# Kernel optimization log

Measured on AMD Instinct MI355X. Metric: run time of the kernel, lower is better.

Reference implementation:

```python
import jax, jax.numpy as jnp
import numpy as np
import math

DIM = 1024
H = 16
D = 64
M = 64  # num_features
B = 1
N = 2048


def _orf_omega(key):
    # Orthogonal Random Features: stack Q^T blocks from QR of Gaussian [D,D]
    blocks = []
    n_blocks = (M + D - 1) // D
    for i in range(n_blocks):
        G = jax.random.normal(jax.random.fold_in(key, i), (D, D), dtype=jnp.float32)
        Q, _ = jnp.linalg.qr(G)
        blocks.append(Q.T)
    return jnp.concatenate(blocks, axis=0)[:M]  # [M, D]


def setup_inputs() -> dict:
    key = jax.random.key(0)
    ks = jax.random.split(key, 7)
    inner = H * D
    x = jax.random.normal(ks[0], (B, N, DIM), dtype=jnp.float32)
    omega = _orf_omega(ks[1])
    wq = jax.random.normal(ks[2], (inner, DIM), dtype=jnp.float32) * 0.02
    wk = jax.random.normal(ks[3], (inner, DIM), dtype=jnp.float32) * 0.02
    wv = jax.random.normal(ks[4], (inner, DIM), dtype=jnp.float32) * 0.02
    wo = jax.random.normal(ks[5], (DIM, inner), dtype=jnp.float32) * 0.02
    bo = jnp.zeros((DIM,), dtype=jnp.float32)
    return {"x": x, "omega": omega, "wq": wq, "wk": wk, "wv": wv, "wo": wo, "bo": bo}


def _phi(x, omega):
    # x: [B,H,N,D], omega: [M,D] -> [B,H,N,M]
    proj = jnp.einsum('bhnd,md->bhnm', x, omega)
    norm = 0.5 * jnp.sum(x * x, axis=-1, keepdims=True)
    return jnp.exp(proj - norm) / math.sqrt(M)


def _heads(t):
    b, n, _ = t.shape
    return t.reshape(b, n, H, D).transpose(0, 2, 1, 3)  # [B,H,N,D]


def reference(x, omega, wq, wk, wv, wo, bo):
    b, n, _ = x.shape
    q = _heads(x @ wq.T)
    k = _heads(x @ wk.T)
    v = _heads(x @ wv.T)
    phi_q = _phi(q, omega)  # [B,H,N,M]
    phi_k = _phi(k, omega)
    # causal linear attention: cumulative KV state (naive materialization, faithful to source)
    kv = jnp.einsum('bhnm,bhnd->bhnmd', phi_k, v)       # [B,H,N,M,D]
    kv_cumsum = jnp.cumsum(kv, axis=2)
    k_cumsum = jnp.cumsum(phi_k, axis=2)                # [B,H,N,M]
    out = jnp.einsum('bhnm,bhnmd->bhnd', phi_q, kv_cumsum)
    z = 1.0 / (jnp.einsum('bhnm,bhnm->bhn', phi_q, k_cumsum) + 1e-6)
    out = out * z[..., None]
    out = out.transpose(0, 2, 1, 3).reshape(b, n, H * D)
    return out @ wo.T + bo
```

## Files before the change

kernel.cpp:

```cpp
#include <hip/hip_runtime.h>
#include <hip/hip_bf16.h>

typedef __hip_bfloat16 bf16;
typedef __attribute__((ext_vector_type(8))) short bf16x8;
typedef __attribute__((ext_vector_type(8))) _Float16 f16x8;
typedef __attribute__((ext_vector_type(4))) float f32x4;

constexpr int N_TOK = 2048;
constexpr int DIMM  = 1024;
constexpr int NH    = 16;
constexpr int HD    = 64;
constexpr int FM    = 64;
constexpr int NC    = 32;
constexpr int CS    = 64;

__device__ __forceinline__ float b2f(bf16 v) { return __bfloat162float(v); }
__device__ __forceinline__ unsigned short f2bfu(float v) {
  bf16 h = __float2bfloat16(v);
  return *reinterpret_cast<unsigned short*>(&h);
}
__device__ __forceinline__ unsigned short f2hu(float v) {
  _Float16 h = (_Float16)v;
  return *reinterpret_cast<unsigned short*>(&h);
}

__device__ __forceinline__ void gl_lds16(const void* g, short* l) {
  __builtin_amdgcn_global_load_lds(
      (const __attribute__((address_space(1))) void*)g,
      (__attribute__((address_space(3))) void*)l, 16, 0, 0);
}

__device__ __forceinline__ void split_pack_bf(const float4 v, uint2& ph, uint2& pl) {
  float f[4] = {v.x, v.y, v.z, v.w};
  unsigned short h[4], l[4];
  #pragma unroll
  for (int j = 0; j < 4; j++) {
    bf16 hb = __float2bfloat16(f[j]);
    h[j] = *reinterpret_cast<unsigned short*>(&hb);
    l[j] = f2bfu(f[j] - b2f(hb));
  }
  ph.x = (unsigned)h[0] | ((unsigned)h[1] << 16);
  ph.y = (unsigned)h[2] | ((unsigned)h[3] << 16);
  pl.x = (unsigned)l[0] | ((unsigned)l[1] << 16);
  pl.y = (unsigned)l[2] | ((unsigned)l[3] << 16);
}

__global__ __launch_bounds__(256) void cvt_all(
    const float4* __restrict__ x, const float4* __restrict__ wq,
    const float4* __restrict__ wk, const float4* __restrict__ wv,
    const float4* __restrict__ wo,
    _Float16* __restrict__ x16, _Float16* __restrict__ w16,
    bf16* __restrict__ wo_bf)
{
  int i = blockIdx.x * 256 + threadIdx.x;
  if (i < 524288) {
    float4 v = x[i];
    uint2 p = { (unsigned)f2hu(v.x) | ((unsigned)f2hu(v.y) << 16),
                (unsigned)f2hu(v.z) | ((unsigned)f2hu(v.w) << 16) };
    reinterpret_cast<uint2*>(x16)[i] = p;
  } else if (i < 1310720) {
    int j = i - 524288;
    const float4* src = (j < 262144) ? wq : (j < 524288) ? wk : wv;
    int jj = (j < 262144) ? j : (j < 524288) ? j - 262144 : j - 524288;
    float4 v = src[jj];
    uint2 p = { (unsigned)f2hu(v.x) | ((unsigned)f2hu(v.y) << 16),
                (unsigned)f2hu(v.z) | ((unsigned)f2hu(v.w) << 16) };
    reinterpret_cast<uint2*>(w16)[j] = p;
  } else {
    int j = i - 1310720;
    float4 v = wo[j];
    uint2 p = { (unsigned)f2bfu(v.x) | ((unsigned)f2bfu(v.y) << 16),
                (unsigned)f2bfu(v.z) | ((unsigned)f2bfu(v.w) << 16) };
    reinterpret_cast<uint2*>(wo_bf)[j] = p;
  }
}

__global__ __launch_bounds__(256) void gemm_qkv_f16(
    const _Float16* __restrict__ A16, const _Float16* __restrict__ B16,
    _Float16* __restrict__ Cq, bf16* __restrict__ Cv)
{
  constexpr int K = 1024;
  __shared__ short sA[2][4096], sB[2][4096];
  const int tid = threadIdx.x, lane = tid & 63, wv = tid >> 6;
  const int colBase = blockIdx.x * 128, rowBase = blockIdx.y * 128;
  const int waveRow = (wv >> 1) * 64, waveCol = (wv & 1) * 64;
  const int stR = tid >> 2, stK = (tid & 3) * 8;

  const _Float16* gA = A16 + (size_t)(rowBase + stR) * K + stK;
  const _Float16* gB = B16 + (size_t)(colBase + stR) * K + stK;
  const int ldsOff0 = wv * 512, ldsOff1 = 2048 + wv * 512;

  f32x4 acc[4][4];
  #pragma unroll
  for (int r = 0; r < 4; r++)
    #pragma unroll
    for (int c = 0; c < 4; c++) acc[r][c] = (f32x4){0.f, 0.f, 0.f, 0.f};

  const int frow = lane & 15, fk = (lane >> 4) * 8;
  const int nIter = K / 32;

  gl_lds16(gA, &sA[0][ldsOff0]); gl_lds16(gA + (size_t)64 * K, &sA[0][ldsOff1]);
  gl_lds16(gB, &sB[0][ldsOff0]); gl_lds16(gB + (size_t)64 * K, &sB[0][ldsOff1]);

  int buf = 0;
  for (int it = 0; it < nIter; it++) {
    __syncthreads();
    if (it + 1 < nIter) {
      const size_t kb = (size_t)(it + 1) * 32;
      const int nb = buf ^ 1;
      gl_lds16(gA + kb, &sA[nb][ldsOff0]); gl_lds16(gA + (size_t)64 * K + kb, &sA[nb][ldsOff1]);
      gl_lds16(gB + kb, &sB[nb][ldsOff0]); gl_lds16(gB + (size_t)64 * K + kb, &sB[nb][ldsOff1]);
    }
    f16x8 a[4], b[4];
    #pragma unroll
    for (int r = 0; r < 4; r++)
      a[r] = *reinterpret_cast<const f16x8*>(&sA[buf][(waveRow + r * 16 + frow) * 32 + fk]);
    #pragma unroll
    for (int c = 0; c < 4; c++)
      b[c] = *reinterpret_cast<const f16x8*>(&sB[buf][(waveCol + c * 16 + frow) * 32 + fk]);
    #pragma unroll
    for (int r = 0; r < 4; r++)
      #pragma unroll
      for (int c = 0; c < 4; c++)
        acc[r][c] = __builtin_amdgcn_mfma_f32_16x16x32_f16(a[r], b[c], acc[r][c], 0, 0, 0);
    buf ^= 1;
  }

  #pragma unroll
  for (int r = 0; r < 4; r++)
    #pragma unroll
    for (int c = 0; c < 4; c++)
      #pragma unroll
      for (int reg = 0; reg < 4; reg++) {
        int row = rowBase + waveRow + r * 16 + (lane >> 4) * 4 + reg;
        int col = colBase + waveCol + c * 16 + (lane & 15);
        float v = acc[r][c][reg];
        if (col < 2048) Cq[(size_t)row * 2048 + col] = (_Float16)v;
        else            Cv[(size_t)row * 1024 + (col - 2048)] = __float2bfloat16(v);
      }
}

__global__ __launch_bounds__(256) void gemm_bf16_out(
    const bf16* __restrict__ A, const bf16* __restrict__ B,
    const float* __restrict__ bias, float* __restrict__ C)
{
  constexpr int K = 1024;
  __shared__ short sA[2][2048], sB[2][4096];
  const int tid = threadIdx.x, lane = tid & 63, wv = tid >> 6;
  const int rowBase = blockIdx.y * 64, colBase = blockIdx.x * 128;
  const int waveRow = (wv >> 1) * 32, waveCol = (wv & 1) * 64;
  const int stR = tid >> 2, stK = (tid & 3) * 8;
  const bf16* gA = A + (size_t)(rowBase + stR) * K + stK;
  const bf16* gB = B + (size_t)(colBase + stR) * K + stK;
  const int ldsOff = wv * 512;

  f32x4 acc[2][4];
  #pragma unroll
  for (int r = 0; r < 2; r++)
    #pragma unroll
    for (int c = 0; c < 4; c++) acc[r][c] = (f32x4){0.f, 0.f, 0.f, 0.f};

  const int frow = lane & 15, fk = (lane >> 4) * 8;
  const int nIter = K / 32;

  gl_lds16(gA, &sA[0][ldsOff]);
  gl_lds16(gB, &sB[0][ldsOff]);
  gl_lds16(gB + (size_t)64 * K, &sB[0][2048 + ldsOff]);

  int buf = 0;
  for (int it = 0; it < nIter; it++) {
    __syncthreads();
    if (it + 1 < nIter) {
      const size_t kb = (size_t)(it + 1) * 32;
      const int nb = buf ^ 1;
      gl_lds16(gA + kb, &sA[nb][ldsOff]);
      gl_lds16(gB + kb, &sB[nb][ldsOff]);
      gl_lds16(gB + (size_t)64 * K + kb, &sB[nb][2048 + ldsOff]);
    }
    bf16x8 a[2], b[4];
    #pragma unroll
    for (int r = 0; r < 2; r++)
      a[r] = *reinterpret_cast<const bf16x8*>(&sA[buf][(waveRow + r * 16 + frow) * 32 + fk]);
    #pragma unroll
    for (int c = 0; c < 4; c++)
      b[c] = *reinterpret_cast<const bf16x8*>(&sB[buf][(waveCol + c * 16 + frow) * 32 + fk]);
    #pragma unroll
    for (int r = 0; r < 2; r++)
      #pragma unroll
      for (int c = 0; c < 4; c++)
        acc[r][c] = __builtin_amdgcn_mfma_f32_16x16x32_bf16(a[r], b[c], acc[r][c], 0, 0, 0);
    buf ^= 1;
  }

  #pragma unroll
  for (int r = 0; r < 2; r++)
    #pragma unroll
    for (int c = 0; c < 4; c++)
      #pragma unroll
      for (int reg = 0; reg < 4; reg++) {
        int row = rowBase + waveRow + r * 16 + (lane >> 4) * 4 + reg;
        int col = colBase + waveCol + c * 16 + (lane & 15);
        C[(size_t)row * 1024 + col] = acc[r][c][reg] + bias[col];
      }
}

__global__ __launch_bounds__(256) void phi_mfma(
    const _Float16* __restrict__ qk, const float* __restrict__ omega,
    bf16* __restrict__ phiq, bf16* __restrict__ phik)
{
  constexpr int LD = 72;
  __shared__ short sAh[128 * LD], sAl[128 * LD];
  __shared__ short sBh[64 * LD],  sBl[64 * LD];
  __shared__ float sPart[128][2];

  const int tid = threadIdx.x, lane = tid & 63, wv = tid >> 6;
  const int n0 = blockIdx.x * 128, h = blockIdx.y, z = blockIdx.z;
  const int colOff = z * 1024 + h * HD;

  {
    const int r = tid >> 1, half = tid & 1;
    const _Float16* src = qk + (size_t)(n0 + r) * 2048 + colOff + half * 32;
    float ssq = 0.f;
    #pragma unroll
    for (int j8 = 0; j8 < 4; j8++) {
      uint4 raw = reinterpret_cast<const uint4*>(src)[j8];
      const unsigned short* hs = reinterpret_cast<const unsigned short*>(&raw);
      unsigned short hh[8], ll[8];
      #pragma unroll
      for (int j = 0; j < 8; j++) {
        _Float16 hv;
        *reinterpret_cast<unsigned short*>(&hv) = hs[j];
        float f = (float)hv;
        ssq += f * f;
        bf16 hb = __float2bfloat16(f);
        hh[j] = *reinterpret_cast<unsigned short*>(&hb);
        ll[j] = f2bfu(f - b2f(hb));
      }
      int o = r * LD + half * 32 + j8 * 8;
      uint4 ph = { (unsigned)hh[0] | ((unsigned)hh[1] << 16),
                   (unsigned)hh[2] | ((unsigned)hh[3] << 16),
                   (unsigned)hh[4] | ((unsigned)hh[5] << 16),
                   (unsigned)hh[6] | ((unsigned)hh[7] << 16) };
      uint4 pl = { (unsigned)ll[0] | ((unsigned)ll[1] << 16),
                   (unsigned)ll[2] | ((unsigned)ll[3] << 16),
                   (unsigned)ll[4] | ((unsigned)ll[5] << 16),
                   (unsigned)ll[6] | ((unsigned)ll[7] << 16) };
      *reinterpret_cast<uint4*>(&sAh[o]) = ph;
      *reinterpret_cast<uint4*>(&sAl[o]) = pl;
    }
    sPart[r][half] = ssq;
  }
  {
    const int r = tid >> 2, q4 = tid & 3;
    const float* src = omega + (size_t)r * FM + q4 * 16;
    #pragma unroll
    for (int j4 = 0; j4 < 4; j4++) {
      float4 v = reinterpret_cast<const float4*>(src)[j4];
      uint2 ph, pl;
      split_pack_bf(v, ph, pl);
      int o = r * LD + q4 * 16 + j4 * 4;
      *reinterpret_cast<uint2*>(&sBh[o]) = ph;
      *reinterpret_cast<uint2*>(&sBl[o]) = pl;
    }
  }
  __syncthreads();

  const int waveRow = (wv >> 1) * 64, waveCol = (wv & 1) * 32;
  const int frow = lane & 15, fk = (lane >> 4) * 8;

  f32x4 acc[4][2];
  #pragma unroll
  for (int r = 0; r < 4; r++)
    #pragma unroll
    for (int c = 0; c < 2; c++) acc[r][c] = (f32x4){0.f, 0.f, 0.f, 0.f};

  #pragma unroll
  for (int ks = 0; ks < 64; ks += 32) {
    bf16x8 ah[4], al[4], bh[2], bl[2];
    #pragma unroll
    for (int r = 0; r < 4; r++) {
      int o = (waveRow + r * 16 + frow) * LD + ks + fk;
      ah[r] = *reinterpret_cast<const bf16x8*>(&sAh[o]);
      al[r] = *reinterpret_cast<const bf16x8*>(&sAl[o]);
    }
    #pragma unroll
    for (int c = 0; c < 2; c++) {
      int o = (waveCol + c * 16 + frow) * LD + ks + fk;
      bh[c] = *reinterpret_cast<const bf16x8*>(&sBh[o]);
      bl[c] = *reinterpret_cast<const bf16x8*>(&sBl[o]);
    }
    #pragma unroll
    for (int r = 0; r < 4; r++)
      #pragma unroll
      for (int c = 0; c < 2; c++) {
        acc[r][c] = __builtin_amdgcn_mfma_f32_16x16x32_bf16(ah[r], bh[c], acc[r][c], 0, 0, 0);
        acc[r][c] = __builtin_amdgcn_mfma_f32_16x16x32_bf16(ah[r], bl[c], acc[r][c], 0, 0, 0);
        acc[r][c] = __builtin_amdgcn_mfma_f32_16x16x32_bf16(al[r], bh[c], acc[r][c], 0, 0, 0);
      }
  }

  bf16* dst = z ? phik : phiq;
  #pragma unroll
  for (int r = 0; r < 4; r++)
    #pragma unroll
    for (int c = 0; c < 2; c++)
      #pragma unroll
      for (int reg = 0; reg < 4; reg++) {
        int row = waveRow + r * 16 + (lane >> 4) * 4 + reg;
        int col = waveCol + c * 16 + (lane & 15);
        float norm = 0.5f * (sPart[row][0] + sPart[row][1]);
        float v = __expf(fminf(acc[r][c][reg] - norm, 80.f)) * 0.125f;
        dst[((size_t)h * N_TOK + n0 + row) * FM + col] = __float2bfloat16(v);
      }
}

__global__ __launch_bounds__(256) void chunk_sum(
    const bf16* __restrict__ phik, const bf16* __restrict__ vf,
    float* __restrict__ ckv, float* __restrict__ ck)
{
  const int c = blockIdx.x, h = blockIdx.y;
  __shared__ float sPk[64][65];
  __shared__ float sV[64][65];
  const int tid = threadIdx.x;
  for (int t = tid; t < 4096; t += 256) {
    int j = t >> 6, e = t & 63;
    sPk[j][e] = b2f(phik[((size_t)h * N_TOK + c * CS + j) * FM + e]);
    sV[j][e]  = b2f(vf[(size_t)(c * CS + j) * DIMM + h * HD + e]);
  }
  __syncthreads();
  const int tx = tid & 15, ty = tid >> 4;
  const int m0 = ty * 4, d0 = tx * 4;
  float acc[4][4] = {};
  for (int j = 0; j < 64; j++) {
    float p[4], v[4];
    #pragma unroll
    for (int u = 0; u < 4; u++) { p[u] = sPk[j][m0 + u]; v[u] = sV[j][d0 + u]; }
    #pragma unroll
    for (int u = 0; u < 4; u++)
      #pragma unroll
      for (int w = 0; w < 4; w++) acc[u][w] += p[u] * v[w];
  }
  float* dst = ckv + ((size_t)h * NC + c) * FM * HD;
  #pragma unroll
  for (int u = 0; u < 4; u++)
    #pragma unroll
    for (int w = 0; w < 4; w++) dst[(m0 + u) * HD + d0 + w] = acc[u][w];
  if (tid < 64) {
    float s = 0.f;
    for (int j = 0; j < 64; j++) s += sPk[j][tid];
    ck[((size_t)h * NC + c) * FM + tid] = s;
  }
}

__global__ __launch_bounds__(256) void prefix_chunks(
    float* __restrict__ ckv, float* __restrict__ ck)
{
  const int h = blockIdx.x, g = blockIdx.y;
  const int cell = g * 256 + threadIdx.x;
  const size_t base = (size_t)h * NC * 4096 + cell;
  float v[NC];
  #pragma unroll
  for (int c = 0; c < NC; c++) v[c] = ckv[base + (size_t)c * 4096];
  float run = 0.f;
  #pragma unroll
  for (int c = 0; c < NC; c++) { float t = v[c]; ckv[base + (size_t)c * 4096] = run; run += t; }
  if (g == 0 && threadIdx.x < 64) {
    const size_t b2 = (size_t)h * NC * FM + threadIdx.x;
    float u[NC];
    #pragma unroll
    for (int c = 0; c < NC; c++) u[c] = ck[b2 + (size_t)c * FM];
    float r2 = 0.f;
    #pragma unroll
    for (int c = 0; c < NC; c++) { float t = u[c]; ck[b2 + (size_t)c * FM] = r2; r2 += t; }
  }
}

__global__ __launch_bounds__(256) void attn_chunk(
    const bf16* __restrict__ phiq, const bf16* __restrict__ phik,
    const bf16* __restrict__ vf, const float* __restrict__ ckv,
    const float* __restrict__ ck, bf16* __restrict__ attn_out)
{
  const int c = blockIdx.x, h = blockIdx.y;
  __shared__ float sPq[64][65];
  __shared__ float sPk[64][65];
  __shared__ float sV[64][65];
  __shared__ float sS[64][65];
  __shared__ float sKc[64];
  __shared__ float sDen[64];
  const int tid = threadIdx.x;
  const float* ckv_base = ckv + ((size_t)h * NC + c) * 4096;
  for (int t = tid; t < 4096; t += 256) {
    int i = t >> 6, e = t & 63;
    sPq[i][e] = b2f(phiq[((size_t)h * N_TOK + c * CS + i) * FM + e]);
    sPk[i][e] = b2f(phik[((size_t)h * N_TOK + c * CS + i) * FM + e]);
    sV[i][e]  = b2f(vf[(size_t)(c * CS + i) * DIMM + h * HD + e]);
    sS[i][e]  = ckv_base[t];
  }
  if (tid < 64) sKc[tid] = ck[((size_t)h * NC + c) * FM + tid];
  __syncthreads();

  const int tx = tid & 15, ty = tid >> 4;
  const int i0 = ty * 4, j0 = tx * 4;

  float accA[4][4] = {};
  for (int m = 0; m < 64; m++) {
    float a[4], b[4];
    #pragma unroll
    for (int u = 0; u < 4; u++) { a[u] = sPq[i0 + u][m]; b[u] = sPk[j0 + u][m]; }
    #pragma unroll
    for (int u = 0; u < 4; u++)
      #pragma unroll
      for (int w = 0; w < 4; w++) accA[u][w] += a[u] * b[w];
  }
  __syncthreads();
  #pragma unroll
  for (int u = 0; u < 4; u++)
    #pragma unroll
    for (int w = 0; w < 4; w++)
      sPk[i0 + u][j0 + w] = (j0 + w <= i0 + u) ? accA[u][w] : 0.f;
  __syncthreads();

  if (tid < 64) {
    float den = 0.f;
    for (int m = 0; m < 64; m++) den += sPq[tid][m] * sKc[m];
    for (int j = 0; j < 64; j++) den += sPk[tid][j];
    sDen[tid] = 1.f / (den + 1e-6f);
  }
  __syncthreads();

  float accO[4][4] = {};
  for (int j = 0; j < 64; j++) {
    float a[4], v[4];
    #pragma unroll
    for (int u = 0; u < 4; u++) { a[u] = sPk[i0 + u][j]; v[u] = sV[j][j0 + u]; }
    #pragma unroll
    for (int u = 0; u < 4; u++)
      #pragma unroll
      for (int w = 0; w < 4; w++) accO[u][w] += a[u] * v[w];
  }
  for (int m = 0; m < 64; m++) {
    float a[4], s[4];
    #pragma unroll
    for (int u = 0; u < 4; u++) { a[u] = sPq[i0 + u][m]; s[u] = sS[m][j0 + u]; }
    #pragma unroll
    for (int u = 0; u < 4; u++)
      #pragma unroll
      for (int w = 0; w < 4; w++) accO[u][w] += a[u] * s[w];
  }
  #pragma unroll
  for (int u = 0; u < 4; u++) {
    int n = c * CS + i0 + u;
    float inv = sDen[i0 + u];
    uint2 pk2;
    pk2.x = (unsigned)f2bfu(accO[u][0] * inv) | ((unsigned)f2bfu(accO[u][1] * inv) << 16);
    pk2.y = (unsigned)f2bfu(accO[u][2] * inv) | ((unsigned)f2bfu(accO[u][3] * inv) << 16);
    *reinterpret_cast<uint2*>(attn_out + (size_t)n * DIMM + h * HD + j0) = pk2;
  }
}

extern "C" void kernel_launch(void* const* d_in, const int* in_sizes, int n_in,
                              void* d_out, int out_size, void* d_ws, size_t ws_size,
                              hipStream_t stream) {
  (void)in_sizes; (void)n_in; (void)out_size; (void)ws_size;
  const float* x     = (const float*)d_in[0];
  const float* omega = (const float*)d_in[1];
  const float* wq    = (const float*)d_in[2];
  const float* wk    = (const float*)d_in[3];
  const float* wv    = (const float*)d_in[4];
  const float* wo    = (const float*)d_in[5];
  const float* bo    = (const float*)d_in[6];
  float* out = (float*)d_out;

  char* w = (char*)d_ws;
  _Float16* x16   = (_Float16*)(w);
  _Float16* w16   = (_Float16*)(w + (4u  << 20));
  bf16*     wo_bf = (bf16*)   (w + (10u << 20));
  _Float16* qk    = (_Float16*)(w + (12u << 20));
  bf16*     vbf   = (bf16*)   (w + (20u << 20));
  bf16*     phiq  = (bf16*)   (w + (24u << 20));
  bf16*     phik  = (bf16*)   (w + (28u << 20));
  float*    ckv   = (float*)  (w + (32u << 20));
  float*    ck    = (float*)  (w + (40u << 20));
  bf16*     attnb = (bf16*)x16;

  cvt_all<<<6144, 256, 0, stream>>>((const float4*)x, (const float4*)wq,
                                    (const float4*)wk, (const float4*)wv,
                                    (const float4*)wo,
                                    x16, w16, wo_bf);

  gemm_qkv_f16<<<dim3(24, 16), 256, 0, stream>>>(x16, w16, qk, vbf);

  phi_mfma<<<dim3(N_TOK / 128, NH, 2), 256, 0, stream>>>(qk, omega, phiq, phik);

  chunk_sum<<<dim3(NC, NH), 256, 0, stream>>>(phik, vbf, ckv, ck);
  prefix_chunks<<<dim3(NH, 16), 256, 0, stream>>>(ckv, ck);
  attn_chunk<<<dim3(NC, NH), 256, 0, stream>>>(phiq, phik, vbf, ckv, ck, attnb);

  gemm_bf16_out<<<dim3(8, 32), 256, 0, stream>>>(attnb, wo_bf, bo, out);
}
```

Measured before the change: 174.3 us.

## Use bf16 MFMA in chunk_sum and attn_chunk with split-precision state

Replaces the scalar FP32 outer-product loops in chunk_sum and attn_chunk with 16x16x32 bf16 MFMA instructions. Operands are staged in padded bf16 shared-memory tiles, some of them transposed. The chunk KV state is now stored transposed as [d][m]. To keep accuracy, the FP32 prefix state and the masked QK^T scores are split into hi/lo bf16 pairs and fed through two MFMAs each, and vectorised uint4 loads replace the scalar loads. The kernels are small compared with the projection GEMMs, so the overall gain is bounded, and bf16 quantisation of phi_q in the state product carries some accuracy risk.

After: 151.7 us. -13.0%, faster.

```diff
diff --git a/kernel.cpp b/kernel.cpp
--- a/kernel.cpp
+++ b/kernel.cpp
@@ -316,40 +316,75 @@
 
 __global__ __launch_bounds__(256) void chunk_sum(
     const bf16* __restrict__ phik, const bf16* __restrict__ vf,
-    float* __restrict__ ckv, float* __restrict__ ck)
-{
+    float* __restrict__ ckv_t, float* __restrict__ ck)
+{
+  constexpr int LD = 72;
+  __shared__ short sVt[64 * LD], sPkt[64 * LD];
+  __shared__ float sCp[64][4];
   const int c = blockIdx.x, h = blockIdx.y;
-  __shared__ float sPk[64][65];
-  __shared__ float sV[64][65];
-  const int tid = threadIdx.x;
-  for (int t = tid; t < 4096; t += 256) {
-    int j = t >> 6, e = t & 63;
-    sPk[j][e] = b2f(phik[((size_t)h * N_TOK + c * CS + j) * FM + e]);
-    sV[j][e]  = b2f(vf[(size_t)(c * CS + j) * DIMM + h * HD + e]);
-  }
-  __syncthreads();
-  const int tx = tid & 15, ty = tid >> 4;
-  const int m0 = ty * 4, d0 = tx * 4;
-  float acc[4][4] = {};
-  for (int j = 0; j < 64; j++) {
-    float p[4], v[4];
-    #pragma unroll
-    for (int u = 0; u < 4; u++) { p[u] = sPk[j][m0 + u]; v[u] = sV[j][d0 + u]; }
-    #pragma unroll
-    for (int u = 0; u < 4; u++)
-      #pragma unroll
-      for (int w = 0; w < 4; w++) acc[u][w] += p[u] * v[w];
-  }
-  float* dst = ckv + ((size_t)h * NC + c) * FM * HD;
-  #pragma unroll
-  for (int u = 0; u < 4; u++)
-    #pragma unroll
-    for (int w = 0; w < 4; w++) dst[(m0 + u) * HD + d0 + w] = acc[u][w];
-  if (tid < 64) {
+  const int tid = threadIdx.x, lane = tid & 63, wv = tid >> 6;
+
+  {
+    int j = tid >> 2, g = tid & 3;
+    const bf16* vs = vf + (size_t)(c * CS + j) * DIMM + h * HD + g * 16;
+    uint4 v0 = *reinterpret_cast<const uint4*>(vs);
+    uint4 v1 = *reinterpret_cast<const uint4*>(vs + 8);
+    const unsigned short* pv = (const unsigned short*)&v0;
+    #pragma unroll
+    for (int e = 0; e < 8; e++) sVt[(g * 16 + e) * LD + j] = (short)pv[e];
+    pv = (const unsigned short*)&v1;
+    #pragma unroll
+    for (int e = 0; e < 8; e++) sVt[(g * 16 + 8 + e) * LD + j] = (short)pv[e];
+
+    const bf16* ks = phik + ((size_t)h * N_TOK + c * CS + j) * FM + g * 16;
+    uint4 k0 = *reinterpret_cast<const uint4*>(ks);
+    uint4 k1 = *reinterpret_cast<const uint4*>(ks + 8);
+    pv = (const unsigned short*)&k0;
+    #pragma unroll
+    for (int e = 0; e < 8; e++) sPkt[(g * 16 + e) * LD + j] = (short)pv[e];
+    pv = (const unsigned short*)&k1;
+    #pragma unroll
+    for (int e = 0; e < 8; e++) sPkt[(g * 16 + 8 + e) * LD + j] = (short)pv[e];
+  }
+  __syncthreads();
+
+  const int frow = lane & 15, fk = (lane >> 4) * 8;
+  const int rowW = wv * 16;
+
+  f32x4 acc[4];
+  #pragma unroll
+  for (int mt = 0; mt < 4; mt++) acc[mt] = (f32x4){0.f, 0.f, 0.f, 0.f};
+  #pragma unroll
+  for (int ks = 0; ks < 64; ks += 32) {
+    bf16x8 a = *reinterpret_cast<const bf16x8*>(&sVt[(rowW + frow) * LD + ks + fk]);
+    #pragma unroll
+    for (int mt = 0; mt < 4; mt++) {
+      bf16x8 b = *reinterpret_cast<const bf16x8*>(&sPkt[(mt * 16 + frow) * LD + ks + fk]);
+      acc[mt] = __builtin_amdgcn_mfma_f32_16x16x32_bf16(a, b, acc[mt], 0, 0, 0);
+    }
+  }
+
+  {
+    int m = tid >> 2, q = tid & 3;
     float s = 0.f;
-    for (int j = 0; j < 64; j++) s += sPk[j][tid];
-    ck[((size_t)h * NC + c) * FM + tid] = s;
-  }
+    #pragma unroll
+    for (int e = 0; e < 16; e++)
+      s += b2f(*reinterpret_cast<bf16*>(&sPkt[m * LD + q * 16 + e]));
+    sCp[m][q] = s;
+  }
+  __syncthreads();
+  if (tid < 64)
+    ck[((size_t)h * NC + c) * FM + tid] = sCp[tid][0] + sCp[tid][1] + sCp[tid][2] + sCp[tid][3];
+
+  float* dst = ckv_t + ((size_t)h * NC + c) * 4096;
+  #pragma unroll
+  for (int mt = 0; mt < 4; mt++)
+    #pragma unroll
+    for (int reg = 0; reg < 4; reg++) {
+      int gd = rowW + (lane >> 4) * 4 + reg;
+      int gm = mt * 16 + (lane & 15);
+      dst[gd * 64 + gm] = acc[mt][reg];
+    }
 }
 
 __global__ __launch_bounds__(256) void prefix_chunks(
@@ -377,85 +412,141 @@
 
 __global__ __launch_bounds__(256) void attn_chunk(
     const bf16* __restrict__ phiq, const bf16* __restrict__ phik,
-    const bf16* __restrict__ vf, const float* __restrict__ ckv,
+    const bf16* __restrict__ vf, const float* __restrict__ ckv_t,
     const float* __restrict__ ck, bf16* __restrict__ attn_out)
 {
+  constexpr int LD = 72;
+  __shared__ short sPq[64 * LD];
+  __shared__ short sPk[64 * LD];
+  __shared__ short sAl[64 * LD];
+  __shared__ short sVt[64 * LD];
+  __shared__ short sSh[64 * LD];
+  __shared__ short sSl[64 * LD];
+  __shared__ float sKc[64];
+  __shared__ float sDp[64][4];
+  __shared__ float sDen[64];
+
   const int c = blockIdx.x, h = blockIdx.y;
-  __shared__ float sPq[64][65];
-  __shared__ float sPk[64][65];
-  __shared__ float sV[64][65];
-  __shared__ float sS[64][65];
-  __shared__ float sKc[64];
-  __shared__ float sDen[64];
-  const int tid = threadIdx.x;
-  const float* ckv_base = ckv + ((size_t)h * NC + c) * 4096;
-  for (int t = tid; t < 4096; t += 256) {
-    int i = t >> 6, e = t & 63;
-    sPq[i][e] = b2f(phiq[((size_t)h * N_TOK + c * CS + i) * FM + e]);
-    sPk[i][e] = b2f(phik[((size_t)h * N_TOK + c * CS + i) * FM + e]);
-    sV[i][e]  = b2f(vf[(size_t)(c * CS + i) * DIMM + h * HD + e]);
-    sS[i][e]  = ckv_base[t];
+  const int tid = threadIdx.x, lane = tid & 63, wv = tid >> 6;
+
+  {
+    int r = tid >> 2, g = tid & 3;
+    const size_t gb = ((size_t)h * N_TOK + c * CS + r) * FM + g * 16;
+    uint4 q0 = *reinterpret_cast<const uint4*>(phiq + gb);
+    uint4 q1 = *reinterpret_cast<const uint4*>(phiq + gb + 8);
+    uint4 k0 = *reinterpret_cast<const uint4*>(phik + gb);
+    uint4 k1 = *reinterpret_cast<const uint4*>(phik + gb + 8);
+    int o = r * LD + g * 16;
+    *reinterpret_cast<uint4*>(&sPq[o]) = q0; *reinterpret_cast<uint4*>(&sPq[o + 8]) = q1;
+    *reinterpret_cast<uint4*>(&sPk[o]) = k0; *reinterpret_cast<uint4*>(&sPk[o + 8]) = k1;
+  }
+  {
+    int j = tid >> 2, g = tid & 3;
+    const bf16* vs = vf + (size_t)(c * CS + j) * DIMM + h * HD + g * 16;
+    uint4 v0 = *reinterpret_cast<const uint4*>(vs);
+    uint4 v1 = *reinterpret_cast<const uint4*>(vs + 8);
+    const unsigned short* pv = (const unsigned short*)&v0;
+    #pragma unroll
+    for (int e = 0; e < 8; e++) sVt[(g * 16 + e) * LD + j] = (short)pv[e];
+    pv = (const unsigned short*)&v1;
+    #pragma unroll
+    for (int e = 0; e < 8; e++) sVt[(g * 16 + 8 + e) * LD + j] = (short)pv[e];
+  }
+  {
+    int d = tid >> 2, mg = tid & 3;
+    const float* src = ckv_t + ((size_t)h * NC + c) * 4096 + d * 64 + mg * 16;
+    int o = d * LD + mg * 16;
+    #pragma unroll
+    for (int e4 = 0; e4 < 4; e4++) {
+      float4 v = *reinterpret_cast<const float4*>(src + e4 * 4);
+      uint2 ph, pl;
+      split_pack_bf(v, ph, pl);
+      *reinterpret_cast<uint2*>(&sSh[o + e4 * 4]) = ph;
+      *reinterpret_cast<uint2*>(&sSl[o + e4 * 4]) = pl;
+    }
   }
   if (tid < 64) sKc[tid] = ck[((size_t)h * NC + c) * FM + tid];
   __syncthreads();
 
-  const int tx = tid & 15, ty = tid >> 4;
-  const int i0 = ty * 4, j0 = tx * 4;
-
-  float accA[4][4] = {};
-  for (int m = 0; m < 64; m++) {
-    float a[4], b[4];
-    #pragma unroll
-    for (int u = 0; u < 4; u++) { a[u] = sPq[i0 + u][m]; b[u] = sPk[j0 + u][m]; }
-    #pragma unroll
-    for (int u = 0; u < 4; u++)
-      #pragma unroll
-      for (int w = 0; w < 4; w++) accA[u][w] += a[u] * b[w];
-  }
-  __syncthreads();
-  #pragma unroll
-  for (int u = 0; u < 4; u++)
-    #pragma unroll
-    for (int w = 0; w < 4; w++)
-      sPk[i0 + u][j0 + w] = (j0 + w <= i0 + u) ? accA[u][w] : 0.f;
-  __syncthreads();
-
+  const int frow = lane & 15, fk = (lane >> 4) * 8;
+  const int rowW = wv * 16;
+
+  f32x4 accA[4];
+  #pragma unroll
+  for (int ct = 0; ct < 4; ct++) accA[ct] = (f32x4){0.f, 0.f, 0.f, 0.f};
+  #pragma unroll
+  for (int ks = 0; ks < 64; ks += 32) {
+    bf16x8 a = *reinterpret_cast<const bf16x8*>(&sPq[(rowW + frow) * LD + ks + fk]);
+    #pragma unroll
+    for (int ct = 0; ct < 4; ct++) {
+      bf16x8 b = *reinterpret_cast<const bf16x8*>(&sPk[(ct * 16 + frow) * LD + ks + fk]);
+      accA[ct] = __builtin_amdgcn_mfma_f32_16x16x32_bf16(a, b, accA[ct], 0, 0, 0);
+    }
+  }
+  __syncthreads();
+
+  #pragma unroll
+  for (int ct = 0; ct < 4; ct++)
+    #pragma unroll
+    for (int reg = 0; reg < 4; reg++) {
+      int gi = rowW + (lane >> 4) * 4 + reg;
+      int gj = ct * 16 + (lane & 15);
+      float av = (gj <= gi) ? accA[ct][reg] : 0.f;
+      bf16 hb = __float2bfloat16(av);
+      sPk[gi * LD + gj] = *reinterpret_cast<short*>(&hb);
+      unsigned short lu = f2bfu(av - b2f(hb));
+      sAl[gi * LD + gj] = (short)lu;
+    }
+  __syncthreads();
+
+  {
+    int i = tid >> 2, q = tid & 3;
+    float p = 0.f;
+    #pragma unroll
+    for (int e = 0; e < 16; e++) {
+      int m = q * 16 + e;
+      p += b2f(*reinterpret_cast<bf16*>(&sPq[i * LD + m])) * sKc[m];
+      p += b2f(*reinterpret_cast<bf16*>(&sPk[i * LD + m]))
+         + b2f(*reinterpret_cast<bf16*>(&sAl[i * LD + m]));
+    }
+    sDp[i][q] = p;
+  }
+
+  f32x4 accO[4];
+  #pragma unroll
+  for (int dt = 0; dt < 4; dt++) accO[dt] = (f32x4){0.f, 0.f, 0.f, 0.f};
+  #pragma unroll
+  for (int ks = 0; ks < 64; ks += 32) {
+    bf16x8 ah = *reinterpret_cast<const bf16x8*>(&sPk[(rowW + frow) * LD + ks + fk]);
+    bf16x8 al = *reinterpret_cast<const bf16x8*>(&sAl[(rowW + frow) * LD + ks + fk]);
+    bf16x8 aq = *reinterpret_cast<const bf16x8*>(&sPq[(rowW + frow) * LD + ks + fk]);
+    #pragma unroll
+    for (int dt = 0; dt < 4; dt++) {
+      bf16x8 bv = *reinterpret_cast<const bf16x8*>(&sVt[(dt * 16 + frow) * LD + ks + fk]);
+      bf16x8 bh = *reinterpret_cast<const bf16x8*>(&sSh[(dt * 16 + frow) * LD + ks + fk]);
+      bf16x8 bl = *reinterpret_cast<const bf16x8*>(&sSl[(dt * 16 + frow) * LD + ks + fk]);
+      accO[dt] = __builtin_amdgcn_mfma_f32_16x16x32_bf16(ah, bv, accO[dt], 0, 0, 0);
+      accO[dt] = __builtin_amdgcn_mfma_f32_16x16x32_bf16(al, bv, accO[dt], 0, 0, 0);
+      accO[dt] = __builtin_amdgcn_mfma_f32_16x16x32_bf16(aq, bh, accO[dt], 0, 0, 0);
+      accO[dt] = __builtin_amdgcn_mfma_f32_16x16x32_bf16(aq, bl, accO[dt], 0, 0, 0);
+    }
+  }
+  __syncthreads();
   if (tid < 64) {
-    float den = 0.f;
-    for (int m = 0; m < 64; m++) den += sPq[tid][m] * sKc[m];
-    for (int j = 0; j < 64; j++) den += sPk[tid][j];
+    float den = sDp[tid][0] + sDp[tid][1] + sDp[tid][2] + sDp[tid][3];
     sDen[tid] = 1.f / (den + 1e-6f);
   }
   __syncthreads();
 
-  float accO[4][4] = {};
-  for (int j = 0; j < 64; j++) {
-    float a[4], v[4];
-    #pragma unroll
-    for (int u = 0; u < 4; u++) { a[u] = sPk[i0 + u][j]; v[u] = sV[j][j0 + u]; }
-    #pragma unroll
-    for (int u = 0; u < 4; u++)
-      #pragma unroll
-      for (int w = 0; w < 4; w++) accO[u][w] += a[u] * v[w];
-  }
-  for (int m = 0; m < 64; m++) {
-    float a[4], s[4];
-    #pragma unroll
-    for (int u = 0; u < 4; u++) { a[u] = sPq[i0 + u][m]; s[u] = sS[m][j0 + u]; }
-    #pragma unroll
-    for (int u = 0; u < 4; u++)
-      #pragma unroll
-      for (int w = 0; w < 4; w++) accO[u][w] += a[u] * s[w];
-  }
-  #pragma unroll
-  for (int u = 0; u < 4; u++) {
-    int n = c * CS + i0 + u;
-    float inv = sDen[i0 + u];
-    uint2 pk2;
-    pk2.x = (unsigned)f2bfu(accO[u][0] * inv) | ((unsigned)f2bfu(accO[u][1] * inv) << 16);
-    pk2.y = (unsigned)f2bfu(accO[u][2] * inv) | ((unsigned)f2bfu(accO[u][3] * inv) << 16);
-    *reinterpret_cast<uint2*>(attn_out + (size_t)n * DIMM + h * HD + j0) = pk2;
-  }
+  #pragma unroll
+  for (int dt = 0; dt < 4; dt++)
+    #pragma unroll
+    for (int reg = 0; reg < 4; reg++) {
+      int gi = rowW + (lane >> 4) * 4 + reg;
+      int gd = dt * 16 + (lane & 15);
+      float v = accO[dt][reg] * sDen[gi];
+      attn_out[(size_t)(c * CS + gi) * DIMM + h * HD + gd] = __float2bfloat16(v);
+    }
 }
 
 extern "C" void kernel_launch(void* const* d_in, const int* in_sizes, int n_in,
```
